# Kernel tuning notes

Measured on AMD Instinct MI355X. Metric: run time of the kernel, lower is better.

Reference implementation:

```python
import jax, jax.numpy as jnp
import numpy as np

B, S, D, Fd, M, H, L = 4, 1024, 1024, 4096, 512, 16, 2
HD = D // H
EPS = 1e-5


def _ln(x, s, b):
    m = jnp.mean(x, axis=-1, keepdims=True)
    v = jnp.mean((x - m) ** 2, axis=-1, keepdims=True)
    return (x - m) * jax.lax.rsqrt(v + EPS) * s + b


def _mha(x, Wq, bq, Wk, bk, Wv, bv, Wo, bo):
    b_, s_, _ = x.shape
    Q = (x @ Wq + bq).reshape(b_, s_, H, HD)
    K = (x @ Wk + bk).reshape(b_, s_, H, HD)
    V = (x @ Wv + bv).reshape(b_, s_, H, HD)
    scores = jnp.einsum('bihd,bjhd->bhij', Q, K) / np.sqrt(HD).astype(np.float32)
    w = jax.nn.softmax(scores, axis=-1)
    out = jnp.einsum('bhij,bjhd->bihd', w, V).reshape(b_, s_, D)
    return out @ Wo + bo


def setup_inputs() -> dict:
    key = jax.random.key(0)
    ks = iter(jax.random.split(key, 40))
    w = lambda shape: jax.random.normal(next(ks), shape, jnp.float32) * 0.02
    inp = {
        'x': jax.random.normal(next(ks), (B, S, D), jnp.float32),
        # stacked per-global-layer params [L, ...]
        'Wq': w((L, D, D)), 'bq': jnp.zeros((L, D)),
        'Wk': w((L, D, D)), 'bk': jnp.zeros((L, D)),
        'Wv': w((L, D, D)), 'bv': jnp.zeros((L, D)),
        'Wo': w((L, D, D)), 'bo': jnp.zeros((L, D)),
        'W1': w((L, D, Fd)), 'b1': jnp.zeros((L, Fd)),
        'W2': w((L, Fd, D)), 'b2': jnp.zeros((L, D)),
        'n1s': jnp.ones((L, D)), 'n1b': jnp.zeros((L, D)),
        'n2s': jnp.ones((L, D)), 'n2b': jnp.zeros((L, D)),
        # top-level params
        'ln1s': jnp.ones((D,)), 'ln1b': jnp.zeros((D,)),
        'ln2s': jnp.ones((D,)), 'ln2b': jnp.zeros((D,)),
        'ln3s': jnp.ones((D,)), 'ln3b': jnp.zeros((D,)),
        'Wb': w((D, M)), 'bb': jnp.zeros((M,)),      # backbone stand-in
        'Wm': w((M, D)), 'bm': jnp.zeros((D,)),      # self.linear
        'Wf1': w((D, Fd)), 'bf1': jnp.zeros((Fd,)),  # top feed_forward
        'Wf2': w((Fd, D)), 'bf2': jnp.zeros((D,)),
    }
    return inp


def reference(x, Wq, bq, Wk, bk, Wv, bv, Wo, bo, W1, b1, W2, b2,
              n1s, n1b, n2s, n2b, ln1s, ln1b, ln2s, ln2b, ln3s, ln3b,
              Wb, bb, Wm, bm, Wf1, bf1, Wf2, bf2):
    # dropout is identity (eval mode)
    # global branch: stacked EncoderLayers
    g = x
    for i in range(L):
        a = _mha(g, Wq[i], bq[i], Wk[i], bk[i], Wv[i], bv[i], Wo[i], bo[i])
        g = _ln(g + a, n1s[i], n1b[i])
        ff = jax.nn.relu(g @ W1[i] + b1[i]) @ W2[i] + b2[i]
        g = _ln(g + ff, n2s[i], n2b[i])

    def local(frac):
        st = S // frac
        xs = x[:, -st:, :]
        mo = (xs @ Wb + bb) @ Wm + bm
        y = _ln(xs + mo, ln1s, ln1b)
        return jnp.pad(y, ((0, 0), (S - st, 0), (0, 0)))

    output = g + local(2) + local(4)  # S >= 4 branch
    h = _ln(output + x, ln2s, ln2b)
    ff = jax.nn.relu(output @ Wf1 + bf1) @ Wf2 + bf2
    return _ln(h + ff, ln3s, ln3b)
```

## Files before the change

### kernel.cpp

```cpp
#include <hip/hip_runtime.h>
#include <stdint.h>


typedef short   s16x8 __attribute__((ext_vector_type(8)));
typedef float   f32x4 __attribute__((ext_vector_type(4)));
typedef uint16_t u16x8 __attribute__((ext_vector_type(8)));
typedef uint16_t u16x4 __attribute__((ext_vector_type(4)));

__device__ __forceinline__ float bf2f(uint16_t h) {
    union { uint32_t u; float f; } c; c.u = ((uint32_t)h) << 16; return c.f;
}
__device__ __forceinline__ uint16_t f2bf(float f) {
    union { float f; uint32_t u; } c; c.f = f;
    uint32_t u = c.u;
    u += 0x7fffu + ((u >> 16) & 1u);
    return (uint16_t)(u >> 16);
}

__device__ __forceinline__ void g2l16(const uint16_t* g, uint16_t* l) {
    __builtin_amdgcn_global_load_lds(
        (const __attribute__((address_space(1))) void*)g,
        (__attribute__((address_space(3))) void*)l, 16, 0, 0);
}

template<int MODE>
__global__ __launch_bounds__(512, 2) void gemm256(
    const uint16_t* __restrict__ A, const uint16_t* __restrict__ Bt,
    const float* __restrict__ bias0, const float* __restrict__ bias1,
    const float* __restrict__ bias2,
    uint16_t* __restrict__ C0, uint16_t* __restrict__ C1,
    uint16_t* __restrict__ C2,
    int N)
{
    __shared__ __align__(16) uint16_t smem[65536];
    uint16_t* sA = smem;
    uint16_t* sB = smem + 32768;

    const int tid  = threadIdx.x;
    const int lane = tid & 63;
    const int w    = tid >> 6;
    const int qd   = lane >> 4;
    const int cc   = lane & 15;
    const int wmg  = w >> 2;
    const int wni  = w & 3;
    const int wn   = wni * 64;
    const int wb   = tid & ~63;

    const int nwg = gridDim.x;
    const int cpx = nwg >> 3;
    const int id  = blockIdx.x;
    const int wg  = (id & 7) * cpx + (id >> 3);
    const int bm  = wg & 15;
    const int bn  = wg >> 4;
    const int m0  = bm * 256;
    const int n0  = bn * 256;

    const float* bp = bias0;
    int n0c = n0;
    if (MODE == 3) {
        int seg = n0 >> 10;
        n0c = n0 & 1023;
        bp = (seg == 0) ? bias0 : (seg == 1) ? bias1 : bias2;
    }
    float bb[4];
#pragma unroll
    for (int j = 0; j < 4; ++j) bb[j] = bp[n0c + wn + j * 16 + cc];

    int offA[8], offB[4];
#pragma unroll
    for (int i = 0; i < 8; ++i) {
        int ml = wmg * 128 + i * 16 + cc;
        offA[i] = ml * 32 + ((qd ^ ((ml >> 1) & 3)) * 8);
    }
#pragma unroll
    for (int j = 0; j < 4; ++j) {
        int nl = wn + j * 16 + cc;
        offB[j] = nl * 32 + ((qd ^ ((nl >> 1) & 3)) * 8);
    }

    int rS[2], kS[2];
#pragma unroll
    for (int is = 0; is < 2; ++is) {
        int gc = is * 512 + tid;
        int row = gc >> 2, ph = gc & 3;
        rS[is] = row;
        kS[is] = (ph ^ ((row >> 1) & 3)) * 8;
    }
    auto stA = [&](int tt) {
        uint16_t* d = sA + (tt & 3) * 8192;
        int kt = tt * 32;
#pragma unroll
        for (int is = 0; is < 2; ++is)
            g2l16(A + (size_t)(m0 + rS[is]) * 1024 + kt + kS[is],
                  d + (size_t)(is * 512 + wb) * 8);
    };
    auto stB = [&](int tt) {
        uint16_t* d = sB + (tt & 3) * 8192;
        int kt = tt * 32;
#pragma unroll
        for (int is = 0; is < 2; ++is)
            g2l16(Bt + (size_t)(n0 + rS[is]) * 1024 + kt + kS[is],
                  d + (size_t)(is * 512 + wb) * 8);
    };

    f32x4 acc[8][4];
#pragma unroll
    for (int i = 0; i < 8; ++i)
#pragma unroll
        for (int j = 0; j < 4; ++j) acc[i][j] = (f32x4)0.0f;

    stA(0); stB(0); stA(1); stB(1); stA(2); stB(2);
    asm volatile("s_waitcnt vmcnt(8)" ::: "memory");
    __builtin_amdgcn_s_barrier();

    s16x8 bv[4];
#pragma unroll 1
    for (int t = 0; t < 32; ++t) {
        const uint16_t* sa = sA + (t & 3) * 8192;
        const uint16_t* sb = sB + (t & 3) * 8192;
        if (t < 29) stA(t + 3);
        s16x8 av[4];
#pragma unroll
        for (int j = 0; j < 4; ++j) bv[j] = *(const s16x8*)(sb + offB[j]);
#pragma unroll
        for (int i = 0; i < 4; ++i) av[i] = *(const s16x8*)(sa + offA[i]);
        __builtin_amdgcn_s_barrier();
        asm volatile("s_waitcnt lgkmcnt(0)" ::: "memory");
        __builtin_amdgcn_sched_barrier(0);
        __builtin_amdgcn_s_setprio(1);
#pragma unroll
        for (int i = 0; i < 4; ++i)
#pragma unroll
            for (int j = 0; j < 4; ++j)
                acc[i][j] = __builtin_amdgcn_mfma_f32_16x16x32_bf16(
                    av[i], bv[j], acc[i][j], 0, 0, 0);
        __builtin_amdgcn_s_setprio(0);
        __builtin_amdgcn_s_barrier();
        if (t < 29) stB(t + 3);
#pragma unroll
        for (int i = 0; i < 4; ++i) av[i] = *(const s16x8*)(sa + offA[4 + i]);
        __builtin_amdgcn_s_barrier();
        asm volatile("s_waitcnt lgkmcnt(0)" ::: "memory");
        __builtin_amdgcn_sched_barrier(0);
        __builtin_amdgcn_s_setprio(1);
#pragma unroll
        for (int i = 0; i < 4; ++i)
#pragma unroll
            for (int j = 0; j < 4; ++j)
                acc[4 + i][j] = __builtin_amdgcn_mfma_f32_16x16x32_bf16(
                    av[i], bv[j], acc[4 + i][j], 0, 0, 0);
        __builtin_amdgcn_s_setprio(0);
        if (t < 29)       { asm volatile("s_waitcnt vmcnt(8)" ::: "memory"); }
        else if (t == 29) { asm volatile("s_waitcnt vmcnt(4)" ::: "memory"); }
        else if (t == 30) { asm volatile("s_waitcnt vmcnt(0)" ::: "memory"); }
        __builtin_amdgcn_s_barrier();
    }

    if (MODE == 3 && (n0 >> 10) == 2) {
#pragma unroll
        for (int j = 0; j < 4; ++j) {
            int c = n0c + wn + j * 16 + cc;
            int hh = c >> 6, d = c & 63;
#pragma unroll
            for (int i = 0; i < 8; ++i) {
                int rb = m0 + wmg * 128 + i * 16 + qd * 4;
                int b = rb >> 10, s = rb & 1023;
                u16x4 o;
#pragma unroll
                for (int r = 0; r < 4; ++r) o[r] = f2bf(acc[i][j][r] + bb[j]);
                *(u16x4*)(C2 + ((size_t)((b * 16 + hh) * 64 + d)) * 1024 + s) = o;
            }
        }
        return;
    }
    {
        uint16_t* C = C0;
        int Nc = N;
        if (MODE == 3) {
            int seg = n0 >> 10;
            C = (seg == 0) ? C0 : C1;
            Nc = 1024;
        }
        constexpr int ST = 264;
#pragma unroll
        for (int h = 0; h < 2; ++h) {
            if (wmg == h) {
#pragma unroll
                for (int i = 0; i < 8; ++i)
#pragma unroll
                    for (int j = 0; j < 4; ++j) {
                        f32x4 v = acc[i][j];
#pragma unroll
                        for (int r = 0; r < 4; ++r) {
                            float val = v[r] + bb[j];
                            if (MODE == 1) val = fmaxf(val, 0.0f);
                            smem[(i * 16 + qd * 4 + r) * ST + wn + j * 16 + cc] =
                                f2bf(val);
                        }
                    }
            }
            __syncthreads();
#pragma unroll
            for (int p = 0; p < 8; ++p) {
                int row  = p * 16 + (tid >> 5);
                int colc = (tid & 31) * 8;
                u16x8 v = *(const u16x8*)(smem + row * ST + colc);
                *(u16x8*)(C + (size_t)(m0 + h * 128 + row) * Nc + n0c + colc) = v;
            }
            __syncthreads();
        }
    }
}

template<int MODE, int BN, int BK, int DB>
__global__ __launch_bounds__(256) void gemm_bt(
    const uint16_t* __restrict__ A, const uint16_t* __restrict__ Bt,
    const float* __restrict__ bias0, const float* __restrict__ bias1,
    const float* __restrict__ bias2,
    uint16_t* __restrict__ C0, uint16_t* __restrict__ C1,
    uint16_t* __restrict__ C2,
    int M, int N, int K)
{
    constexpr int JN   = BN / 32;
    constexpr int KS   = BK / 32;
    constexpr int CPR  = BK / 8;
    constexpr int LG   = (BK == 32) ? 2 : 3;
    constexpr int RA   = (128 * BK / 8) / 256;
    constexpr int RB   = (BN  * BK / 8) / 256;
    constexpr int NBUF = DB ? 2 : 1;
    constexpr int STG  = NBUF * (128 + BN) * BK;
    constexpr int EPI  = (MODE == 3) ? 0 : 128 * (BN + 8);
    constexpr int SMEM = (STG > EPI) ? STG : EPI;
    __shared__ __align__(16) uint16_t smem[SMEM];
    uint16_t* sAp = smem;
    uint16_t* sBp = smem + NBUF * 128 * BK;

    const int t    = threadIdx.x;
    const int w    = t >> 6;
    const int lane = t & 63;
    const int qd   = lane >> 4;
    const int cc   = lane & 15;

    int bm, bn;
    {
        int gx = gridDim.x, gy = gridDim.y;
        if ((gy & 7) == 0) {
            int id   = blockIdx.y * gx + blockIdx.x;
            int gpg  = gy >> 3;
            int rest = id >> 3;
            bm = (id & 7) * gpg + rest % gpg;
            bn = rest / gpg;
        } else { bm = blockIdx.y; bn = blockIdx.x; }
    }
    const int m0 = bm * 128;
    const int n0 = bn * BN;
    const int wm = (w >> 1) * 64;
    const int wn = (w & 1) * (BN / 2);

    auto key = [](int row) -> int {
        return (BK == 32) ? ((row >> 1) & 3) : (row & 7);
    };

    f32x4 acc[4][JN];
#pragma unroll
    for (int i = 0; i < 4; ++i)
#pragma unroll
        for (int j = 0; j < JN; ++j) acc[i][j] = (f32x4)0.0f;

    int rA[RA], kA[RA];
#pragma unroll
    for (int is = 0; is < RA; ++is) {
        int gc = is * 256 + t;
        int row = gc >> LG, ph = gc & (CPR - 1);
        rA[is] = row;
        kA[is] = (ph ^ key(row)) * 8;
    }
    int rB[RB], kB[RB];
#pragma unroll
    for (int is = 0; is < RB; ++is) {
        int gc = is * 256 + t;
        int row = gc >> LG, ph = gc & (CPR - 1);
        rB[is] = row;
        kB[is] = (ph ^ key(row)) * 8;
    }
    int offA[4][KS], offB[JN][KS];
#pragma unroll
    for (int i = 0; i < 4; ++i) {
        int ml = wm + i * 16 + cc;
#pragma unroll
        for (int ks = 0; ks < KS; ++ks)
            offA[i][ks] = ml * BK + ((ks * 4 + qd) ^ key(ml)) * 8;
    }
#pragma unroll
    for (int j = 0; j < JN; ++j) {
        int nl = wn + j * 16 + cc;
#pragma unroll
        for (int ks = 0; ks < KS; ++ks)
            offB[j][ks] = nl * BK + ((ks * 4 + qd) ^ key(nl)) * 8;
    }

    auto stage = [&](int kt, int buf) {
#pragma unroll
        for (int is = 0; is < RA; ++is)
            g2l16(A + (size_t)(m0 + rA[is]) * K + kt + kA[is],
                  sAp + (size_t)buf * 128 * BK + (size_t)(is * 256 + w * 64) * 8);
#pragma unroll
        for (int is = 0; is < RB; ++is)
            g2l16(Bt + (size_t)(n0 + rB[is]) * K + kt + kB[is],
                  sBp + (size_t)buf * BN * BK + (size_t)(is * 256 + w * 64) * 8);
    };
    auto compute = [&](int buf) {
        const uint16_t* sa = sAp + (size_t)buf * 128 * BK;
        const uint16_t* sb = sBp + (size_t)buf * BN * BK;
#pragma unroll
        for (int ks = 0; ks < KS; ++ks) {
            s16x8 af[4], bv[JN];
#pragma unroll
            for (int i = 0; i < 4; ++i) af[i] = *(const s16x8*)(sa + offA[i][ks]);
#pragma unroll
            for (int j = 0; j < JN; ++j) bv[j] = *(const s16x8*)(sb + offB[j][ks]);
#pragma unroll
            for (int i = 0; i < 4; ++i)
#pragma unroll
                for (int j = 0; j < JN; ++j)
                    acc[i][j] = __builtin_amdgcn_mfma_f32_16x16x32_bf16(
                        af[i], bv[j], acc[i][j], 0, 0, 0);
        }
    };

    if (DB) {
        stage(0, 0);
        __syncthreads();
        int cur = 0;
        for (int kt = 0; kt < K; kt += BK) {
            if (kt + BK < K) stage(kt + BK, cur ^ 1);
            compute(cur);
            __syncthreads();
            cur ^= 1;
        }
    } else {
        for (int kt = 0; kt < K; kt += BK) {
            stage(kt, 0);
            __syncthreads();
            compute(0);
            __syncthreads();
        }
    }

    if (MODE == 3) {
#pragma unroll
        for (int j = 0; j < JN; ++j) {
            int col = n0 + wn + j * 16 + cc;
            int seg = col >> 10;
            const float* bp = (seg == 0) ? bias0 : (seg == 1) ? bias1 : bias2;
            float bb = bp[col & 1023];
#pragma unroll
            for (int i = 0; i < 4; ++i) {
                f32x4 v = acc[i][j];
#pragma unroll
                for (int r = 0; r < 4; ++r) {
                    float val = v[r] + bb;
                    int row = m0 + wm + i * 16 + qd * 4 + r;
                    if (col < 1024) {
                        C0[(size_t)row * 1024 + col] = f2bf(val);
                    } else if (col < 2048) {
                        C1[(size_t)row * 1024 + (col - 1024)] = f2bf(val);
                    } else {
                        int c = col - 2048;
                        int b = row >> 10, s = row & 1023;
                        int hh = c >> 6, d = c & 63;
                        C2[((size_t)(b * 16 + hh) * 64 + d) * 1024 + s] = f2bf(val);
                    }
                }
            }
        }
    } else {
        constexpr int ST = BN + 8;
#pragma unroll
        for (int j = 0; j < JN; ++j) {
            int col = wn + j * 16 + cc;
            float bb = bias0[n0 + col];
#pragma unroll
            for (int i = 0; i < 4; ++i) {
                f32x4 v = acc[i][j];
#pragma unroll
                for (int r = 0; r < 4; ++r) {
                    float val = v[r] + bb;
                    if (MODE == 1) val = fmaxf(val, 0.0f);
                    smem[(wm + i * 16 + qd * 4 + r) * ST + col] = f2bf(val);
                }
            }
        }
        __syncthreads();
        constexpr int NP  = 128 * BN / 2048;
        constexpr int TPR = BN / 8;
#pragma unroll
        for (int p = 0; p < NP; ++p) {
            int row  = p * (256 / TPR) + t / TPR;
            int colc = (t % TPR) * 8;
            u16x8 v = *(const u16x8*)(smem + row * ST + colc);
            *(u16x8*)(C0 + (size_t)(m0 + row) * N + n0 + colc) = v;
        }
    }
}

#define FA_P 76
__global__ __launch_bounds__(256) void flash_attn(
    const uint16_t* __restrict__ Q, const uint16_t* __restrict__ K,
    const uint16_t* __restrict__ Vt, uint16_t* __restrict__ O)
{
    __shared__ __align__(16) uint16_t Qs[64 * FA_P];
    __shared__ __align__(16) uint16_t Ks[64 * FA_P];
    __shared__ __align__(16) uint16_t Vs[64 * FA_P];
    __shared__ __align__(16) uint16_t Ps[64 * FA_P];

    const int t    = threadIdx.x;
    const int w    = t >> 6;
    const int lane = t & 63;
    const int qd   = lane >> 4;
    const int cc   = lane & 15;
    const int id   = blockIdx.x;
    const int xg   = id & 7;
    const int loc  = id >> 3;
    const int bh   = xg * 8 + (loc >> 4);
    const int qblk = loc & 15;
    const int b    = bh >> 4, hh = bh & 15;
    const size_t rowbase = (size_t)b * 1024;

#pragma unroll
    for (int is = 0; is < 2; ++is) {
        int c = is * 256 + t, r = c >> 3, ch = c & 7;
        *(u16x8*)(Qs + r * FA_P + ch * 8) =
            *(const u16x8*)(Q + (rowbase + qblk * 64 + r) * 1024 + hh * 64 + ch * 8);
    }

    f32x4 o[4];
    float lrow[4] = {0.0f, 0.0f, 0.0f, 0.0f};
#pragma unroll
    for (int j = 0; j < 4; ++j) o[j] = (f32x4)0.0f;

    for (int kb = 0; kb < 1024; kb += 64) {
        __syncthreads();
#pragma unroll
        for (int is = 0; is < 2; ++is) {
            int c = is * 256 + t, r = c >> 3, ch = c & 7;
            *(u16x8*)(Ks + r * FA_P + ch * 8) =
                *(const u16x8*)(K + (rowbase + kb + r) * 1024 + hh * 64 + ch * 8);
            *(u16x8*)(Vs + r * FA_P + ch * 8) =
                *(const u16x8*)(Vt + ((size_t)(bh * 64 + r)) * 1024 + kb + ch * 8);
        }
        __syncthreads();

        f32x4 sc[4];
        s16x8 aq0 = *(const s16x8*)(Qs + (w * 16 + cc) * FA_P + qd * 8);
        s16x8 aq1 = *(const s16x8*)(Qs + (w * 16 + cc) * FA_P + 32 + qd * 8);
#pragma unroll
        for (int j = 0; j < 4; ++j) {
            s16x8 b0 = *(const s16x8*)(Ks + (j * 16 + cc) * FA_P + qd * 8);
            s16x8 b1 = *(const s16x8*)(Ks + (j * 16 + cc) * FA_P + 32 + qd * 8);
            sc[j] = __builtin_amdgcn_mfma_f32_16x16x32_bf16(aq0, b0, (f32x4)0.0f, 0, 0, 0);
            sc[j] = __builtin_amdgcn_mfma_f32_16x16x32_bf16(aq1, b1, sc[j], 0, 0, 0);
        }

#pragma unroll
        for (int r = 0; r < 4; ++r) {
            float p0 = __expf(sc[0][r] * 0.125f);
            float p1 = __expf(sc[1][r] * 0.125f);
            float p2 = __expf(sc[2][r] * 0.125f);
            float p3 = __expf(sc[3][r] * 0.125f);
            lrow[r] += (p0 + p1) + (p2 + p3);
            int prow = (w * 16 + qd * 4 + r) * FA_P + cc;
            Ps[prow]      = f2bf(p0);
            Ps[prow + 16] = f2bf(p1);
            Ps[prow + 32] = f2bf(p2);
            Ps[prow + 48] = f2bf(p3);
        }

#pragma unroll
        for (int ks = 0; ks < 2; ++ks) {
            s16x8 ap = *(const s16x8*)(Ps + (w * 16 + cc) * FA_P + ks * 32 + qd * 8);
#pragma unroll
            for (int j = 0; j < 4; ++j) {
                s16x8 bb = *(const s16x8*)(Vs + (j * 16 + cc) * FA_P + ks * 32 + qd * 8);
                o[j] = __builtin_amdgcn_mfma_f32_16x16x32_bf16(ap, bb, o[j], 0, 0, 0);
            }
        }
    }

#pragma unroll
    for (int r = 0; r < 4; ++r) {
        float rs = lrow[r];
        rs += __shfl_xor(rs, 1);
        rs += __shfl_xor(rs, 2);
        rs += __shfl_xor(rs, 4);
        rs += __shfl_xor(rs, 8);
        float inv = 1.0f / rs;
        size_t grow = rowbase + qblk * 64 + w * 16 + qd * 4 + r;
#pragma unroll
        for (int j = 0; j < 4; ++j)
            O[grow * 1024 + hh * 64 + j * 16 + cc] = f2bf(o[j][r] * inv);
    }
}

template<int BT, int F32OUT>
__global__ __launch_bounds__(256) void ln_res(
    const uint16_t* __restrict__ A, const void* __restrict__ Bp,
    const float* __restrict__ S, const float* __restrict__ Bi,
    void* __restrict__ outp)
{
    const int row = blockIdx.x, t = threadIdx.x;
    const int w = t >> 6, lane = t & 63;
    u16x4 a4 = *(const u16x4*)(A + (size_t)row * 1024 + t * 4);
    float bvals[4];
    if (BT == 0) {
        u16x4 b4 = *(const u16x4*)((const uint16_t*)Bp + (size_t)row * 1024 + t * 4);
#pragma unroll
        for (int e = 0; e < 4; ++e) bvals[e] = bf2f(b4[e]);
    } else {
        float4 b4 = *(const float4*)((const float*)Bp + (size_t)row * 1024 + t * 4);
        bvals[0] = b4.x; bvals[1] = b4.y; bvals[2] = b4.z; bvals[3] = b4.w;
    }
    float v[4], sum = 0.0f, sq = 0.0f;
#pragma unroll
    for (int e = 0; e < 4; ++e) {
        v[e] = bf2f(a4[e]) + bvals[e];
        sum += v[e];
        sq  += v[e] * v[e];
    }
#pragma unroll
    for (int d = 1; d < 64; d <<= 1) {
        sum += __shfl_xor(sum, d);
        sq  += __shfl_xor(sq, d);
    }
    __shared__ float rs[4], rq[4];
    if (lane == 0) { rs[w] = sum; rq[w] = sq; }
    __syncthreads();
    sum = rs[0] + rs[1] + rs[2] + rs[3];
    sq  = rq[0] + rq[1] + rq[2] + rq[3];
    float mean = sum * (1.0f / 1024.0f);
    float var  = sq * (1.0f / 1024.0f) - mean * mean;
    float rstd = rsqrtf(var + 1e-5f);
    float4 s4  = *(const float4*)(S + t * 4);
    float4 bi4 = *(const float4*)(Bi + t * 4);
    float r0 = (v[0] - mean) * rstd * s4.x + bi4.x;
    float r1 = (v[1] - mean) * rstd * s4.y + bi4.y;
    float r2 = (v[2] - mean) * rstd * s4.z + bi4.z;
    float r3 = (v[3] - mean) * rstd * s4.w + bi4.w;
    if (F32OUT) {
        *(float4*)((float*)outp + (size_t)row * 1024 + t * 4) =
            make_float4(r0, r1, r2, r3);
    } else {
        u16x4 o4;
        o4[0] = f2bf(r0); o4[1] = f2bf(r1); o4[2] = f2bf(r2); o4[3] = f2bf(r3);
        *(u16x4*)((uint16_t*)outp + (size_t)row * 1024 + t * 4) = o4;
    }
}

__global__ __launch_bounds__(256) void add3(
    const uint16_t* __restrict__ g, const uint16_t* __restrict__ y2,
    const uint16_t* __restrict__ y4, uint16_t* __restrict__ out)
{
    size_t e = ((size_t)blockIdx.x * 256 + threadIdx.x) * 4;
    int row = (int)(e >> 10), col = (int)(e & 1023);
    int b = row >> 10, s = row & 1023;
    u16x4 gv = *(const u16x4*)(g + e);
    float v[4];
#pragma unroll
    for (int k = 0; k < 4; ++k) v[k] = bf2f(gv[k]);
    if (s >= 512) {
        u16x4 a = *(const u16x4*)(y2 + ((size_t)(b * 512 + s - 512)) * 1024 + col);
#pragma unroll
        for (int k = 0; k < 4; ++k) v[k] += bf2f(a[k]);
    }
    if (s >= 768) {
        u16x4 a = *(const u16x4*)(y4 + ((size_t)(b * 256 + s - 768)) * 1024 + col);
#pragma unroll
        for (int k = 0; k < 4; ++k) v[k] += bf2f(a[k]);
    }
    u16x4 o4;
#pragma unroll
    for (int k = 0; k < 4; ++k) o4[k] = f2bf(v[k]);
    *(u16x4*)(out + e) = o4;
}

__global__ __launch_bounds__(256) void copy_rows_f32(
    const float* __restrict__ x, uint16_t* __restrict__ out, int lgst)
{
    size_t e = ((size_t)blockIdx.x * 256 + threadIdx.x) * 4;
    int row = (int)(e >> 10), col = (int)(e & 1023);
    int st = 1 << lgst;
    int b = row >> lgst, s = row & (st - 1);
    float4 a = *(const float4*)(x + ((size_t)(b * 1024 + (1024 - st) + s)) * 1024 + col);
    u16x4 o4;
    o4[0] = f2bf(a.x); o4[1] = f2bf(a.y); o4[2] = f2bf(a.z); o4[3] = f2bf(a.w);
    *(u16x4*)(out + e) = o4;
}

__global__ __launch_bounds__(256) void transpose_k(
    const float* __restrict__ W, uint16_t* __restrict__ Wt, int Kd, int Nd)
{
    __shared__ uint16_t tile[64][68];
    const int t  = threadIdx.x;
    const int n0 = blockIdx.x * 64, k0 = blockIdx.y * 64;
#pragma unroll
    for (int p = 0; p < 4; ++p) {
        int k  = p * 16 + (t >> 4);
        int nn = (t & 15) * 4;
        float4 a = *(const float4*)(W + (size_t)(k0 + k) * Nd + n0 + nn);
        tile[nn + 0][k] = f2bf(a.x);
        tile[nn + 1][k] = f2bf(a.y);
        tile[nn + 2][k] = f2bf(a.z);
        tile[nn + 3][k] = f2bf(a.w);
    }
    __syncthreads();
#pragma unroll
    for (int p = 0; p < 2; ++p) {
        int nn = p * 32 + (t >> 3);
        int kk = (t & 7) * 8;
        u16x8 o = *(const u16x8*)(&tile[nn][kk]);
        *(u16x8*)(Wt + (size_t)(n0 + nn) * Kd + k0 + kk) = o;
    }
}

__global__ __launch_bounds__(256) void cvt(
    const float* __restrict__ src, uint16_t* __restrict__ dst)
{
    size_t i = ((size_t)blockIdx.x * 256 + threadIdx.x) * 8;
    float4 a = *(const float4*)(src + i);
    float4 b = *(const float4*)(src + i + 4);
    u16x8 o;
    o[0] = f2bf(a.x); o[1] = f2bf(a.y); o[2] = f2bf(a.z); o[3] = f2bf(a.w);
    o[4] = f2bf(b.x); o[5] = f2bf(b.y); o[6] = f2bf(b.z); o[7] = f2bf(b.w);
    *(u16x8*)(dst + i) = o;
}

extern "C" void kernel_launch(void* const* d_in, const int* in_sizes, int n_in,
                              void* d_out, int out_size, void* d_ws, size_t ws_size,
                              hipStream_t stream)
{
    const float* x    = (const float*)d_in[0];
    const float* Wq   = (const float*)d_in[1];
    const float* bq   = (const float*)d_in[2];
    const float* Wk   = (const float*)d_in[3];
    const float* bk   = (const float*)d_in[4];
    const float* Wv   = (const float*)d_in[5];
    const float* bv   = (const float*)d_in[6];
    const float* Wo   = (const float*)d_in[7];
    const float* bo   = (const float*)d_in[8];
    const float* W1   = (const float*)d_in[9];
    const float* b1   = (const float*)d_in[10];
    const float* W2   = (const float*)d_in[11];
    const float* b2   = (const float*)d_in[12];
    const float* n1s  = (const float*)d_in[13];
    const float* n1b  = (const float*)d_in[14];
    const float* n2s  = (const float*)d_in[15];
    const float* n2b  = (const float*)d_in[16];
    const float* ln1s = (const float*)d_in[17];
    const float* ln1b = (const float*)d_in[18];
    const float* ln2s = (const float*)d_in[19];
    const float* ln2b = (const float*)d_in[20];
    const float* ln3s = (const float*)d_in[21];
    const float* ln3b = (const float*)d_in[22];
    const float* Wb   = (const float*)d_in[23];
    const float* bb   = (const float*)d_in[24];
    const float* Wm   = (const float*)d_in[25];
    const float* bm   = (const float*)d_in[26];
    const float* Wf1  = (const float*)d_in[27];
    const float* bf1  = (const float*)d_in[28];
    const float* Wf2  = (const float*)d_in[29];
    const float* bf2  = (const float*)d_in[30];

    char* ws = (char*)d_ws;
    const size_t MB = (size_t)1 << 20;
    uint16_t* g    = (uint16_t*)(ws);
    uint16_t* tb   = (uint16_t*)(ws + 8 * MB);
    char*     big  = ws + 16 * MB;
    uint16_t* qb   = (uint16_t*)(big);
    uint16_t* kbuf = (uint16_t*)(big + 8 * MB);
    uint16_t* vtb  = (uint16_t*)(big + 16 * MB);
    uint16_t* ob   = (uint16_t*)(big + 24 * MB);
    uint16_t* ffb  = (uint16_t*)(big);
    uint16_t* xbf  = (uint16_t*)(ws + 48 * MB);
    uint16_t* hb   = (uint16_t*)(ws + 48 * MB);
    uint16_t* wT   = (uint16_t*)(ws + 56 * MB);

    auto T = [&](const float* Wsrc, int Kd, int Nd, uint16_t* dst) {
        transpose_k<<<dim3(Nd / 64, Kd / 64), 256, 0, stream>>>(Wsrc, dst, Kd, Nd);
    };

    cvt<<<2048, 256, 0, stream>>>(x, xbf);

    const uint16_t* gin = xbf;
    for (int i = 0; i < 2; ++i) {
        const size_t wOff = (size_t)i * 1024 * 1024;
        const size_t fOff = (size_t)i * 1024 * 4096;
        T(Wq + wOff, 1024, 1024, wT);
        T(Wk + wOff, 1024, 1024, wT + (size_t)1024 * 1024);
        T(Wv + wOff, 1024, 1024, wT + (size_t)2048 * 1024);
        gemm256<3><<<192, 512, 0, stream>>>(
            gin, wT, bq + i * 1024, bk + i * 1024, bv + i * 1024,
            qb, kbuf, vtb, 3072);
        flash_attn<<<1024, 256, 0, stream>>>(qb, kbuf, vtb, ob);
        T(Wo + wOff, 1024, 1024, wT);
        gemm_bt<0, 64, 64, 1><<<dim3(16, 32), 256, 0, stream>>>(
            ob, wT, bo + i * 1024, nullptr, nullptr, tb, nullptr, nullptr,
            4096, 1024, 1024);
        ln_res<0, 0><<<4096, 256, 0, stream>>>(gin, tb, n1s + i * 1024, n1b + i * 1024, g);
        T(W1 + fOff, 1024, 4096, wT);
        gemm256<1><<<256, 512, 0, stream>>>(
            g, wT, b1 + i * 4096, nullptr, nullptr, ffb, nullptr, nullptr, 4096);
        T(W2 + fOff, 4096, 1024, wT);
        gemm_bt<0, 64, 64, 1><<<dim3(16, 32), 256, 0, stream>>>(
            ffb, wT, b2 + i * 1024, nullptr, nullptr, tb, nullptr, nullptr,
            4096, 1024, 4096);
        ln_res<0, 0><<<4096, 256, 0, stream>>>(g, tb, n2s + i * 1024, n2b + i * 1024, g);
        gin = g;
    }

    uint16_t* xsc = (uint16_t*)(big);
    uint16_t* lk  = (uint16_t*)(big + 8 * MB);
    uint16_t* mo  = (uint16_t*)(big + 16 * MB);
    uint16_t* yy  = (uint16_t*)(big + 24 * MB);
    copy_rows_f32<<<2048, 256, 0, stream>>>(x, xsc, 9);
    copy_rows_f32<<<1024, 256, 0, stream>>>(x, xsc + (size_t)2048 * 1024, 8);
    uint16_t* WbT = wT;
    uint16_t* WmT = wT + (size_t)512 * 1024;
    T(Wb, 1024, 512, WbT);
    T(Wm, 512, 1024, WmT);
    gemm_bt<0, 64, 64, 1><<<dim3(8, 24), 256, 0, stream>>>(
        xsc, WbT, bb, nullptr, nullptr, lk, nullptr, nullptr, 3072, 512, 1024);
    gemm_bt<0, 64, 64, 1><<<dim3(16, 24), 256, 0, stream>>>(
        lk, WmT, bm, nullptr, nullptr, mo, nullptr, nullptr, 3072, 1024, 512);
    ln_res<0, 0><<<3072, 256, 0, stream>>>(xsc, mo, ln1s, ln1b, yy);
    uint16_t* y2 = yy;
    uint16_t* y4 = yy + (size_t)2048 * 1024;

    add3<<<4096, 256, 0, stream>>>(g, y2, y4, g);
    ln_res<1, 0><<<4096, 256, 0, stream>>>(g, x, ln2s, ln2b, hb);
    T(Wf1, 1024, 4096, wT);
    gemm256<1><<<256, 512, 0, stream>>>(
        g, wT, bf1, nullptr, nullptr, ffb, nullptr, nullptr, 4096);
    T(Wf2, 4096, 1024, wT);
    gemm_bt<0, 64, 64, 1><<<dim3(16, 32), 256, 0, stream>>>(
        ffb, wT, bf2, nullptr, nullptr, tb, nullptr, nullptr, 4096, 1024, 4096);
    ln_res<0, 1><<<4096, 256, 0, stream>>>(hb, tb, ln3s, ln3b, d_out);
}
```

Before: 800.4 us.

## Replace 256x256 GEMM tile with 128x256 tile, 4 waves, 3-stage pipeline

The large-tile GEMM used for the fused QKV projection and the FFN up-projections is reworked from 256x256 tiles with 8 waves into 128x256 tiles with 4 waves. Each wave now computes all 8 M-subtiles in one MFMA block per k-step, and loads go through a 3-slot ring instead of 4 slots split into A and B phases. This doubles the number of workgroups (384 and 512), giving better fill across the CUs, and lowers LDS use per block. The cost is less operand reuse per block, more B-tile global traffic, and fewer intra-iteration barriers to overlap loads with MFMA.

Measured after the change: 762.6 us. -4.7%, faster.

```diff
diff --git a/kernel.cpp b/kernel.cpp
--- a/kernel.cpp
+++ b/kernel.cpp
@@ -24,7 +24,7 @@
 }
 
 template<int MODE>
-__global__ __launch_bounds__(512, 2) void gemm256(
+__global__ __launch_bounds__(256, 2) void gemm128n(
     const uint16_t* __restrict__ A, const uint16_t* __restrict__ Bt,
     const float* __restrict__ bias0, const float* __restrict__ bias1,
     const float* __restrict__ bias2,
@@ -32,27 +32,22 @@
     uint16_t* __restrict__ C2,
     int N)
 {
-    __shared__ __align__(16) uint16_t smem[65536];
+    __shared__ __align__(16) uint16_t smem[36864];
     uint16_t* sA = smem;
-    uint16_t* sB = smem + 32768;
-
-    const int tid  = threadIdx.x;
-    const int lane = tid & 63;
-    const int w    = tid >> 6;
+    uint16_t* sB = smem + 12288;
+
+    const int t    = threadIdx.x;
+    const int w    = t >> 6;
+    const int lane = t & 63;
     const int qd   = lane >> 4;
     const int cc   = lane & 15;
-    const int wmg  = w >> 2;
-    const int wni  = w & 3;
-    const int wn   = wni * 64;
-    const int wb   = tid & ~63;
-
-    const int nwg = gridDim.x;
-    const int cpx = nwg >> 3;
+    const int wn   = w * 64;
+
     const int id  = blockIdx.x;
-    const int wg  = (id & 7) * cpx + (id >> 3);
-    const int bm  = wg & 15;
-    const int bn  = wg >> 4;
-    const int m0  = bm * 256;
+    const int loc = id >> 3;
+    const int bm  = (id & 7) * 4 + (loc & 3);
+    const int bn  = loc >> 2;
+    const int m0  = bm * 128;
     const int n0  = bn * 256;
 
     const float* bp = bias0;
@@ -69,7 +64,7 @@
     int offA[8], offB[4];
 #pragma unroll
     for (int i = 0; i < 8; ++i) {
-        int ml = wmg * 128 + i * 16 + cc;
+        int ml = i * 16 + cc;
         offA[i] = ml * 32 + ((qd ^ ((ml >> 1) & 3)) * 8);
     }
 #pragma unroll
@@ -78,30 +73,31 @@
         offB[j] = nl * 32 + ((qd ^ ((nl >> 1) & 3)) * 8);
     }
 
-    int rS[2], kS[2];
+    const uint16_t* pA[2]; int ldA[2];
 #pragma unroll
     for (int is = 0; is < 2; ++is) {
-        int gc = is * 512 + tid;
+        int gc = is * 256 + t;
         int row = gc >> 2, ph = gc & 3;
-        rS[is] = row;
-        kS[is] = (ph ^ ((row >> 1) & 3)) * 8;
-    }
-    auto stA = [&](int tt) {
-        uint16_t* d = sA + (tt & 3) * 8192;
+        pA[is]  = A + (size_t)(m0 + row) * 1024 + (ph ^ ((row >> 1) & 3)) * 8;
+        ldA[is] = (is * 256 + w * 64) * 8;
+    }
+    const uint16_t* pB[4]; int ldB[4];
+#pragma unroll
+    for (int is = 0; is < 4; ++is) {
+        int gc = is * 256 + t;
+        int row = gc >> 2, ph = gc & 3;
+        pB[is]  = Bt + (size_t)(n0 + row) * 1024 + (ph ^ ((row >> 1) & 3)) * 8;
+        ldB[is] = (is * 256 + w * 64) * 8;
+    }
+    auto stage = [&](int tt, int slot) {
         int kt = tt * 32;
-#pragma unroll
-        for (int is = 0; is < 2; ++is)
-            g2l16(A + (size_t)(m0 + rS[is]) * 1024 + kt + kS[is],
-                  d + (size_t)(is * 512 + wb) * 8);
+        uint16_t* dA = sA + slot * 4096;
+        uint16_t* dB = sB + slot * 8192;
+#pragma unroll
+        for (int is = 0; is < 2; ++is) g2l16(pA[is] + kt, dA + ldA[is]);
+#pragma unroll
+        for (int is = 0; is < 4; ++is) g2l16(pB[is] + kt, dB + ldB[is]);
     };
-    auto stB = [&](int tt) {
-        uint16_t* d = sB + (tt & 3) * 8192;
-        int kt = tt * 32;
-#pragma unroll
-        for (int is = 0; is < 2; ++is)
-            g2l16(Bt + (size_t)(n0 + rS[is]) * 1024 + kt + kS[is],
-                  d + (size_t)(is * 512 + wb) * 8);
-    };
 
     f32x4 acc[8][4];
 #pragma unroll
@@ -109,51 +105,36 @@
 #pragma unroll
         for (int j = 0; j < 4; ++j) acc[i][j] = (f32x4)0.0f;
 
-    stA(0); stB(0); stA(1); stB(1); stA(2); stB(2);
-    asm volatile("s_waitcnt vmcnt(8)" ::: "memory");
+    stage(0, 0); stage(1, 1);
+    asm volatile("s_waitcnt vmcnt(6)" ::: "memory");
     __builtin_amdgcn_s_barrier();
 
-    s16x8 bv[4];
+    int cur = 0, pf = 2;
 #pragma unroll 1
-    for (int t = 0; t < 32; ++t) {
-        const uint16_t* sa = sA + (t & 3) * 8192;
-        const uint16_t* sb = sB + (t & 3) * 8192;
-        if (t < 29) stA(t + 3);
-        s16x8 av[4];
+    for (int kt = 0; kt < 32; ++kt) {
+        const uint16_t* sa = sA + cur * 4096;
+        const uint16_t* sb = sB + cur * 8192;
+        s16x8 av[8], bv[4];
 #pragma unroll
         for (int j = 0; j < 4; ++j) bv[j] = *(const s16x8*)(sb + offB[j]);
 #pragma unroll
-        for (int i = 0; i < 4; ++i) av[i] = *(const s16x8*)(sa + offA[i]);
-        __builtin_amdgcn_s_barrier();
+        for (int i = 0; i < 8; ++i) av[i] = *(const s16x8*)(sa + offA[i]);
+        if (kt < 30) stage(kt + 2, pf);
         asm volatile("s_waitcnt lgkmcnt(0)" ::: "memory");
         __builtin_amdgcn_sched_barrier(0);
         __builtin_amdgcn_s_setprio(1);
 #pragma unroll
-        for (int i = 0; i < 4; ++i)
+        for (int i = 0; i < 8; ++i)
 #pragma unroll
             for (int j = 0; j < 4; ++j)
                 acc[i][j] = __builtin_amdgcn_mfma_f32_16x16x32_bf16(
                     av[i], bv[j], acc[i][j], 0, 0, 0);
         __builtin_amdgcn_s_setprio(0);
+        if (kt < 30)       { asm volatile("s_waitcnt vmcnt(6)" ::: "memory"); }
+        else if (kt == 30) { asm volatile("s_waitcnt vmcnt(0)" ::: "memory"); }
         __builtin_amdgcn_s_barrier();
-        if (t < 29) stB(t + 3);
-#pragma unroll
-        for (int i = 0; i < 4; ++i) av[i] = *(const s16x8*)(sa + offA[4 + i]);
-        __builtin_amdgcn_s_barrier();
-        asm volatile("s_waitcnt lgkmcnt(0)" ::: "memory");
-        __builtin_amdgcn_sched_barrier(0);
-        __builtin_amdgcn_s_setprio(1);
-#pragma unroll
-        for (int i = 0; i < 4; ++i)
-#pragma unroll
-            for (int j = 0; j < 4; ++j)
-                acc[4 + i][j] = __builtin_amdgcn_mfma_f32_16x16x32_bf16(
-                    av[i], bv[j], acc[4 + i][j], 0, 0, 0);
-        __builtin_amdgcn_s_setprio(0);
-        if (t < 29)       { asm volatile("s_waitcnt vmcnt(8)" ::: "memory"); }
-        else if (t == 29) { asm volatile("s_waitcnt vmcnt(4)" ::: "memory"); }
-        else if (t == 30) { asm volatile("s_waitcnt vmcnt(0)" ::: "memory"); }
-        __builtin_amdgcn_s_barrier();
+        pf = cur;
+        cur = (cur == 2) ? 0 : cur + 1;
     }
 
     if (MODE == 3 && (n0 >> 10) == 2) {
@@ -163,7 +144,7 @@
             int hh = c >> 6, d = c & 63;
 #pragma unroll
             for (int i = 0; i < 8; ++i) {
-                int rb = m0 + wmg * 128 + i * 16 + qd * 4;
+                int rb = m0 + i * 16 + qd * 4;
                 int b = rb >> 10, s = rb & 1023;
                 u16x4 o;
 #pragma unroll
@@ -183,31 +164,24 @@
         }
         constexpr int ST = 264;
 #pragma unroll
-        for (int h = 0; h < 2; ++h) {
-            if (wmg == h) {
-#pragma unroll
-                for (int i = 0; i < 8; ++i)
-#pragma unroll
-                    for (int j = 0; j < 4; ++j) {
-                        f32x4 v = acc[i][j];
-#pragma unroll
-                        for (int r = 0; r < 4; ++r) {
-                            float val = v[r] + bb[j];
-                            if (MODE == 1) val = fmaxf(val, 0.0f);
-                            smem[(i * 16 + qd * 4 + r) * ST + wn + j * 16 + cc] =
-                                f2bf(val);
-                        }
-                    }
+        for (int i = 0; i < 8; ++i)
+#pragma unroll
+            for (int j = 0; j < 4; ++j) {
+                f32x4 v = acc[i][j];
+#pragma unroll
+                for (int r = 0; r < 4; ++r) {
+                    float val = v[r] + bb[j];
+                    if (MODE == 1) val = fmaxf(val, 0.0f);
+                    smem[(i * 16 + qd * 4 + r) * ST + wn + j * 16 + cc] = f2bf(val);
+                }
             }
-            __syncthreads();
-#pragma unroll
-            for (int p = 0; p < 8; ++p) {
-                int row  = p * 16 + (tid >> 5);
-                int colc = (tid & 31) * 8;
-                u16x8 v = *(const u16x8*)(smem + row * ST + colc);
-                *(u16x8*)(C + (size_t)(m0 + h * 128 + row) * Nc + n0c + colc) = v;
-            }
-            __syncthreads();
+        __syncthreads();
+#pragma unroll
+        for (int p = 0; p < 16; ++p) {
+            int row  = p * 8 + (t >> 5);
+            int colc = (t & 31) * 8;
+            u16x8 v = *(const u16x8*)(smem + row * ST + colc);
+            *(u16x8*)(C + (size_t)(m0 + row) * Nc + n0c + colc) = v;
         }
     }
 }
@@ -697,7 +671,7 @@
         T(Wq + wOff, 1024, 1024, wT);
         T(Wk + wOff, 1024, 1024, wT + (size_t)1024 * 1024);
         T(Wv + wOff, 1024, 1024, wT + (size_t)2048 * 1024);
-        gemm256<3><<<192, 512, 0, stream>>>(
+        gemm128n<3><<<384, 256, 0, stream>>>(
             gin, wT, bq + i * 1024, bk + i * 1024, bv + i * 1024,
             qb, kbuf, vtb, 3072);
         flash_attn<<<1024, 256, 0, stream>>>(qb, kbuf, vtb, ob);
@@ -707,7 +681,7 @@
             4096, 1024, 1024);
         ln_res<0, 0><<<4096, 256, 0, stream>>>(gin, tb, n1s + i * 1024, n1b + i * 1024, g);
         T(W1 + fOff, 1024, 4096, wT);
-        gemm256<1><<<256, 512, 0, stream>>>(
+        gemm128n<1><<<512, 256, 0, stream>>>(
             g, wT, b1 + i * 4096, nullptr, nullptr, ffb, nullptr, nullptr, 4096);
         T(W2 + fOff, 4096, 1024, wT);
         gemm_bt<0, 64, 64, 1><<<dim3(16, 32), 256, 0, stream>>>(
@@ -738,7 +712,7 @@
     add3<<<4096, 256, 0, stream>>>(g, y2, y4, g);
     ln_res<1, 0><<<4096, 256, 0, stream>>>(g, x, ln2s, ln2b, hb);
     T(Wf1, 1024, 4096, wT);
-    gemm256<1><<<256, 512, 0, stream>>>(
+    gemm128n<1><<<512, 256, 0, stream>>>(
         g, wT, bf1, nullptr, nullptr, ffb, nullptr, nullptr, 4096);
     T(Wf2, 4096, 1024, wT);
     gemm_bt<0, 64, 64, 1><<<dim3(16, 32), 256, 0, stream>>>(
```
